# Optimization experiments

Measured on AMD Instinct MI355X. Metric: run time of the kernel, lower is better.

Reference implementation:

```python
import jax, jax.numpy as jnp
import numpy as np

SPATIAL_PATH = np.array([[1,0,1],[0,1,2],[1,2,1],[4,3,1],[5,4,3],[6,5,4],[5,6,5],[8,7,1],[9,8,7],[10,9,8],[9,10,9]], dtype=np.int32)

B, C_IN, J, T, C_OUT = 64, 3, 11, 512, 128
TEMPORAL_LEN = 7
SIG_CH = 84  # c = C_IN + 1 = 4 -> 4 + 16 + 64


def _signature_depth3(path):
    """Depth-3 path signature with basepoint=0 (Chen's identity over exp of increments).
    path: [N, L, c] -> [N, c + c^2 + c^3]."""
    N, L, c = path.shape
    # basepoint=True: path starts at 0, so first increment is path[:, 0]
    inc = jnp.concatenate([path[:, :1], path[:, 1:] - path[:, :-1]], axis=1)  # [N, L, c]

    def step(carry, d):
        S1, S2, S3 = carry
        e2 = 0.5 * d[:, :, None] * d[:, None, :]                                  # d^{x2}/2!
        e3 = (d[:, :, None, None] * d[:, None, :, None] * d[:, None, None, :]) / 6.0  # d^{x3}/3!
        T1 = S1 + d
        T2 = S2 + S1[:, :, None] * d[:, None, :] + e2
        T3 = (S3 + S2[:, :, :, None] * d[:, None, None, :]
              + S1[:, :, None, None] * e2[:, None, :, :] + e3)
        return (T1, T2, T3), None

    z = lambda *s: jnp.zeros(s, path.dtype)
    (S1, S2, S3), _ = jax.lax.scan(step, (z(N, c), z(N, c, c), z(N, c, c, c)),
                                   jnp.swapaxes(inc, 0, 1))
    return jnp.concatenate([S1, S2.reshape(N, -1), S3.reshape(N, -1)], axis=1)


def _augment_time(path):
    # signatory.Augment(include_time=True, include_original=True): prepend linear time channel
    N, L, _ = path.shape
    t = jnp.broadcast_to(jnp.linspace(0.0, 1.0, L, dtype=path.dtype)[None, :, None], (N, L, 1))
    return jnp.concatenate([t, path], axis=-1)


def _bn(x, gamma, beta, eps=1e-5):
    # train-mode BatchNorm2d (batch statistics), matching module default mode
    m = x.mean(axis=(0, 2, 3), keepdims=True)
    v = x.var(axis=(0, 2, 3), keepdims=True)
    return (x - m) * jax.lax.rsqrt(v + eps) * gamma[None, :, None, None] + beta[None, :, None, None]


def _conv1x1(x, w, b):
    return jnp.einsum('bcjt,oc->bojt', x, w) + b[None, :, None, None]


def _forward(x, path, raw_w, raw_b, raw_g, raw_beta,
             ps_w, ps_b, ps_g, ps_beta, fus_w, fus_b, fus_g, fus_beta):
    B_, C, J_, T_ = x.shape
    # raw branch: Conv2d(C_in, C_out, (1,3), pad (0,1)) + BN + ReLU
    x_conv = jax.lax.conv_general_dilated(x, raw_w, (1, 1), [(0, 0), (1, 1)],
                                          dimension_numbers=('NCHW', 'OIHW', 'NCHW'))
    x_conv = jax.nn.relu(_bn(x_conv + raw_b[None, :, None, None], raw_g, raw_beta))

    # spatial joint paths: gather along joint dim with hand-crafted path [J, 3]
    xp = x.transpose(0, 1, 3, 2)                  # [B, C, T, J]
    sp = xp[:, :, :, path]                        # [B, C, T, J, 3]
    sp = sp.transpose(0, 2, 3, 4, 1).reshape(-1, path.shape[1], C)  # [B*T*J, 3, C]
    s_sig = _signature_depth3(_augment_time(sp))
    s_sig = s_sig.reshape(B_, T_, J_, SIG_CH).transpose(0, 3, 2, 1)  # [B, 84, J, T]

    # temporal paths: replicate-pad T and take 7-wide sliding windows per joint
    pad = (TEMPORAL_LEN - 1) // 2
    x_pad = jnp.pad(x, ((0, 0), (0, 0), (0, 0), (pad, pad)), mode='edge')
    widx = jnp.arange(T_)[:, None] + jnp.arange(TEMPORAL_LEN)[None, :]  # [T, 7]
    tp = x_pad[:, :, :, widx]                     # [B, C, J, T, 7]
    tp = tp.transpose(0, 3, 2, 4, 1).reshape(-1, TEMPORAL_LEN, C)       # [B*T*J, 7, C]
    t_sig = _signature_depth3(_augment_time(tp))
    t_sig = t_sig.reshape(B_, T_, J_, SIG_CH).transpose(0, 3, 2, 1)     # [B, 84, J, T]

    sig = jnp.concatenate([s_sig, t_sig], axis=1)                       # [B, 168, J, T]
    sig = jax.nn.relu(_bn(_conv1x1(sig, ps_w, ps_b), ps_g, ps_beta))    # [B, C_out, J, T]

    out = jnp.concatenate([x_conv, sig], axis=1)                        # [B, 2*C_out, J, T]
    return jax.nn.relu(_bn(_conv1x1(out, fus_w, fus_b), fus_g, fus_beta))


def setup_inputs() -> dict:
    key = jax.random.key(0)
    ks = jax.random.split(key, 4)
    return {
        'x': jax.random.normal(ks[0], (B, C_IN, J, T), jnp.float32),
        'path': jnp.asarray(SPATIAL_PATH),
        'raw_w': jax.random.normal(ks[1], (C_OUT, C_IN, 1, 3), jnp.float32) * 0.2,
        'raw_b': jnp.zeros((C_OUT,), jnp.float32),
        'raw_g': jnp.ones((C_OUT,), jnp.float32),
        'raw_beta': jnp.zeros((C_OUT,), jnp.float32),
        'ps_w': jax.random.normal(ks[2], (C_OUT, 2 * SIG_CH), jnp.float32) * 0.05,
        'ps_b': jnp.zeros((C_OUT,), jnp.float32),
        'ps_g': jnp.ones((C_OUT,), jnp.float32),
        'ps_beta': jnp.zeros((C_OUT,), jnp.float32),
        'fus_w': jax.random.normal(ks[3], (C_OUT, 2 * C_OUT), jnp.float32) * 0.05,
        'fus_b': jnp.zeros((C_OUT,), jnp.float32),
        'fus_g': jnp.ones((C_OUT,), jnp.float32),
        'fus_beta': jnp.zeros((C_OUT,), jnp.float32),
    }


def reference(x, path, raw_w, raw_b, raw_g, raw_beta, ps_w, ps_b, ps_g, ps_beta,
              fus_w, fus_b, fus_g, fus_beta):
    return _forward(x, path, raw_w, raw_b, raw_g, raw_beta,
                    ps_w, ps_b, ps_g, ps_beta, fus_w, fus_b, fus_g, fus_beta)
```

## Files before the change

kernel.cpp:

```cpp
#include <hip/hip_runtime.h>

#define B_    64
#define CIN_  3
#define J_    11
#define T_    512
#define CO_   128
#define KPS_  168
#define KPAD_ 192
#define NLOC_ (B_*J_*T_)
#define NSTATF_ 360448.0f

typedef unsigned short u16;
typedef unsigned int   u32;

typedef __attribute__((ext_vector_type(8))) short bh8;
typedef __attribute__((ext_vector_type(4))) float f32x4;

__device__ __forceinline__ float b2f(u16 u){ union{u32 i; float f;} v; v.i = ((u32)u)<<16; return v.f; }
__device__ __forceinline__ u16 f2b(float f){ union{float f; u32 i;} v; v.f=f; u32 r = v.i + 0x7FFFu + ((v.i>>16)&1u); return (u16)(r>>16); }
__device__ __forceinline__ u32 pk2(u16 a, u16 b){ return (u32)a | ((u32)b<<16); }

__device__ __forceinline__ float ldx(const void* p, size_t i, bool bf){
  if (bf) return b2f(((const u16*)p)[i]);
  return ((const float*)p)[i];
}
__device__ __forceinline__ bool rflag(const u32* flag){
  return __builtin_amdgcn_readfirstlane(*flag) != 0u;
}

__global__ void kdet(const u32* __restrict__ xw, u32* __restrict__ flag){
  __shared__ int cnt;
  if (threadIdx.x==0) cnt=0;
  __syncthreads();
  u32 w = xw[threadIdx.x*4 + 1];
  int e = (int)((w>>7)&0xFFu);
  if (e>=100 && e<=140) atomicAdd(&cnt,1);
  __syncthreads();
  if (threadIdx.x==0) *flag = (cnt>128) ? 1u : 0u;
}

__global__ __launch_bounds__(256) void k0_prep(const u32* __restrict__ flag,
    const void* __restrict__ ps_w, const void* __restrict__ fus_w,
    u16* __restrict__ psB, u16* __restrict__ fusB,
    float* __restrict__ statsY, float* __restrict__ statsF)
{
  const bool bf = rflag(flag);
  const int stride = gridDim.x*blockDim.x;
  const int t0 = blockIdx.x*blockDim.x + threadIdx.x;
  for (int i=t0;i<64*512;i+=stride) statsY[i]=0.f;
  for (int i=t0;i<64*256;i+=stride) statsF[i]=0.f;
  for (int i=t0;i<128*KPAD_;i+=stride){
    int o=i/KPAD_, kk=i-o*KPAD_;
    int k = (kk<84) ? kk : ((kk>=96 && kk<180) ? kk-12 : -1);
    psB[i] = (k>=0) ? f2b(ldx(ps_w, (size_t)o*KPS_+k, bf)) : (u16)0;
  }
  for (int i=t0;i<128*256;i+=stride){
    int o=i>>8, k=i&255;
    int kc=k>>6, kk=k&63;
    int byte=(o<<7)+(kk<<1); byte ^= ((o&7)<<4);
    fusB[(kc*16384 + byte)>>1] = f2b(ldx(fus_w,i,bf));
  }
}

__device__ __forceinline__ void sigstep(float* S1, float* S2, float* S3, const float* d){
  float e2[16];
  #pragma unroll
  for (int a=0;a<4;a++){
    #pragma unroll
    for (int b=0;b<4;b++) e2[a*4+b] = 0.5f*d[a]*d[b];
  }
  #pragma unroll
  for (int a=0;a<4;a++){
    float s1e = S1[a] + (1.0f/3.0f)*d[a];
    #pragma unroll
    for (int b=0;b<4;b++){
      #pragma unroll
      for (int c=0;c<4;c++){
        S3[a*16+b*4+c] += S2[a*4+b]*d[c] + s1e*e2[b*4+c];
      }
    }
  }
  #pragma unroll
  for (int a=0;a<4;a++){
    #pragma unroll
    for (int b=0;b<4;b++) S2[a*4+b] += S1[a]*d[b] + e2[a*4+b];
  }
  #pragma unroll
  for (int a=0;a<4;a++) S1[a] += d[a];
}

__global__ __launch_bounds__(256) void k1_sig_conv(const u32* __restrict__ flag,
    const void* __restrict__ x, const int* __restrict__ path,
    const void* __restrict__ raw_w, const void* __restrict__ raw_b,
    const void* __restrict__ ps_b, const u16* __restrict__ psB,
    u16* __restrict__ Y, float* __restrict__ statsY,
    int locOff, int writeY, int doStats)
{
  const bool bf = rflag(flag);
  __shared__ u16 sAhi[64*KPAD_];
  __shared__ u16 sAlo[64*KPAD_];
  __shared__ float xt[CIN_][72];
  __shared__ float xs[CIN_][3][64];
  __shared__ int   pj[3];

  const int tid = threadIdx.x;
  const int blk = blockIdx.x;
  const int lb  = locOff + blk*64;
  const int lbl = blk*64;
  const int b   = lb / (J_*T_);
  const int j   = (lb / T_) % J_;
  const int t0  = lb % T_;
  const size_t xbase = (size_t)b*CIN_*J_*T_;

  if (tid < 3) pj[tid] = path[j*3 + tid];
  for (int idx=tid; idx<CIN_*70; idx+=256){
    int c=idx/70, u=idx-c*70;
    int t=t0+u-3; t = t<0?0:(t>T_-1?T_-1:t);
    xt[c][u] = ldx(x, xbase + (size_t)(c*J_+j)*T_ + t, bf);
  }
  __syncthreads();
  for (int idx=tid; idx<CIN_*3*64; idx+=256){
    int c=idx/192, p=(idx>>6)%3, tt=idx&63;
    xs[c][p][tt] = ldx(x, xbase + (size_t)(c*J_+pj[p])*T_ + t0 + tt, bf);
  }
  __syncthreads();

  const int lane = tid & 63, wid = tid >> 6;
  const int wid2 = wid ^ ((blk&1)<<1);

  if (wid2 < 2){
    const bool spf = (wid2==0);
    const int  tt  = lane;
    const int  L   = spf ? 3 : 7;
    const float dt = spf ? 0.5f : (1.0f/6.0f);
    float S1[4], S2[16], S3[64];
    #pragma unroll
    for (int i=0;i<4;i++)  S1[i]=0.f;
    #pragma unroll
    for (int i=0;i<16;i++) S2[i]=0.f;
    #pragma unroll
    for (int i=0;i<64;i++) S3[i]=0.f;
    float prv[3], d[4];
    for (int c=0;c<3;c++) prv[c] = spf ? xs[c][0][tt] : xt[c][tt];
    d[0]=0.f; d[1]=prv[0]; d[2]=prv[1]; d[3]=prv[2];
    sigstep(S1,S2,S3,d);
    for (int s=1;s<L;s++){
      d[0]=dt;
      for (int c=0;c<3;c++){ float cv = spf ? xs[c][s][tt] : xt[c][tt+s]; d[c+1]=cv-prv[c]; prv[c]=cv; }
      sigstep(S1,S2,S3,d);
    }
    const int sb2 = spf ? 0 : 192;
    const int rowb = tt*(KPAD_*2);
    const int swz  = (tt&7)<<4;
    #pragma unroll
    for (int i=0;i<12;i++){
      u16 hv[8], lv[8];
      #pragma unroll
      for (int e=0;e<8;e++){
        const int idx = i*8+e;
        float v;
        if (idx<4) v=S1[idx]; else if (idx<20) v=S2[idx-4]; else if (idx<84) v=S3[idx-20]; else v=0.f;
        u16 h = f2b(v);
        hv[e]=h; lv[e]=f2b(v - b2f(h));
      }
      int byp = (rowb + sb2 + i*16) ^ swz;
      *reinterpret_cast<uint4*>((char*)sAhi + byp) =
          make_uint4(pk2(hv[0],hv[1]),pk2(hv[2],hv[3]),pk2(hv[4],hv[5]),pk2(hv[6],hv[7]));
      *reinterpret_cast<uint4*>((char*)sAlo + byp) =
          make_uint4(pk2(lv[0],lv[1]),pk2(lv[2],lv[3]),pk2(lv[4],lv[5]),pk2(lv[6],lv[7]));
    }
  } else {
    const int nid = (wid2-2)*64 + lane;
    const int tx = nid & 7, ty2 = nid >> 3;
    #pragma unroll
    for (int cg=0; cg<2; cg++){
      const int chb = cg*64 + ty2*4;
      float w[4][9], bia[4];
      #pragma unroll
      for (int c=0;c<4;c++){
        bia[c]=ldx(raw_b, chb+c, bf);
        #pragma unroll
        for (int q=0;q<9;q++) w[c][q]=ldx(raw_w, (size_t)(chb+c)*9+q, bf);
      }
      float accC[8][4];
      #pragma unroll
      for (int i=0;i<8;i++){
        const int tl=tx*8+i, tg=t0+tl;
        float xv[9];
        #pragma unroll
        for (int cc=0;cc<3;cc++){
          #pragma unroll
          for (int kt=0;kt<3;kt++){
            float v = xt[cc][tl+2+kt];
            if ((tg==0 && kt==0) || (tg==T_-1 && kt==2)) v=0.f;
            xv[cc*3+kt]=v;
          }
        }
        #pragma unroll
        for (int c=0;c<4;c++){
          float s=bia[c];
          #pragma unroll
          for (int q=0;q<9;q++) s=fmaf(xv[q],w[c][q],s);
          accC[i][c]=s;
        }
      }
      if (writeY){
        #pragma unroll
        for (int i=0;i<8;i++){
          u16* yp = Y + (size_t)(lbl + tx*8+i)*256 + chb;
          *reinterpret_cast<uint2*>(yp) =
            make_uint2(pk2(f2b(accC[i][0]),f2b(accC[i][1])), pk2(f2b(accC[i][2]),f2b(accC[i][3])));
        }
      }
      if (doStats){
        #pragma unroll
        for (int c=0;c<4;c++){
          float s=0.f,q=0.f;
          #pragma unroll
          for (int i=0;i<8;i++){ float v=accC[i][c]; s+=v; q+=v*v; }
          s += __shfl_xor(s,1); s += __shfl_xor(s,2); s += __shfl_xor(s,4);
          q += __shfl_xor(q,1); q += __shfl_xor(q,2); q += __shfl_xor(q,4);
          if ((lane&7)==0){
            atomicAdd(&statsY[(blk&63)*512 + (chb+c)*2 + 0], s);
            atomicAdd(&statsY[(blk&63)*512 + (chb+c)*2 + 1], q);
          }
        }
      }
    }
  }
  __syncthreads();

  const int lrow = lane >> 4, lcol = lane & 15;
  f32x4 acc[2][4];
  #pragma unroll
  for (int mt=0;mt<2;mt++)
    #pragma unroll
    for (int nt=0;nt<4;nt++) acc[mt][nt] = (f32x4){0.f,0.f,0.f,0.f};

  #pragma unroll
  for (int ks=0;ks<6;ks++){
    const int kk2 = ks*64 + lrow*16;
    bh8 wf[2], yh[4], yl[4];
    #pragma unroll
    for (int mt=0;mt<2;mt++){
      const int o = wid*32 + mt*16 + lcol;
      wf[mt] = *reinterpret_cast<const bh8*>((const char*)psB + o*(KPAD_*2) + kk2);
    }
    #pragma unroll
    for (int nt=0;nt<4;nt++){
      const int l = nt*16 + lcol;
      const int byp = (l*(KPAD_*2) + kk2) ^ ((l&7)<<4);
      yh[nt] = *reinterpret_cast<const bh8*>((const char*)sAhi + byp);
      yl[nt] = *reinterpret_cast<const bh8*>((const char*)sAlo + byp);
    }
    #pragma unroll
    for (int mt=0;mt<2;mt++){
      #pragma unroll
      for (int nt=0;nt<4;nt++){
        acc[mt][nt] = __builtin_amdgcn_mfma_f32_16x16x32_bf16(wf[mt], yh[nt], acc[mt][nt], 0,0,0);
        acc[mt][nt] = __builtin_amdgcn_mfma_f32_16x16x32_bf16(wf[mt], yl[nt], acc[mt][nt], 0,0,0);
      }
    }
  }
  __syncthreads();

  char* yPs = (char*)sAhi;
  #pragma unroll
  for (int mt=0;mt<2;mt++){
    const int chb = wid*32 + mt*16 + lrow*4;
    float pb[4];
    #pragma unroll
    for (int r=0;r<4;r++) pb[r]=ldx(ps_b, chb+r, bf);
    float sv[4]={0.f,0.f,0.f,0.f}, qv[4]={0.f,0.f,0.f,0.f};
    #pragma unroll
    for (int nt=0;nt<4;nt++){
      const int loc = nt*16 + lcol;
      float v0=acc[mt][nt][0]+pb[0], v1=acc[mt][nt][1]+pb[1];
      float v2=acc[mt][nt][2]+pb[2], v3=acc[mt][nt][3]+pb[3];
      sv[0]+=v0; qv[0]+=v0*v0; sv[1]+=v1; qv[1]+=v1*v1;
      sv[2]+=v2; qv[2]+=v2*v2; sv[3]+=v3; qv[3]+=v3*v3;
      if (writeY){
        const int byp = (loc*256 + chb*2) ^ ((loc&7)<<4);
        *reinterpret_cast<uint2*>(yPs + byp) =
            make_uint2(pk2(f2b(v0),f2b(v1)), pk2(f2b(v2),f2b(v3)));
      }
    }
    if (doStats){
      #pragma unroll
      for (int r=0;r<4;r++){
        float s=sv[r], q=qv[r];
        s += __shfl_xor(s,1); s += __shfl_xor(s,2); s += __shfl_xor(s,4); s += __shfl_xor(s,8);
        q += __shfl_xor(q,1); q += __shfl_xor(q,2); q += __shfl_xor(q,4); q += __shfl_xor(q,8);
        if (lcol==0){
          const int ch = 128 + chb + r;
          atomicAdd(&statsY[(blk&63)*512 + ch*2 + 0], s);
          atomicAdd(&statsY[(blk&63)*512 + ch*2 + 1], q);
        }
      }
    }
  }
  __syncthreads();
  if (writeY){
    #pragma unroll
    for (int it=0; it<4; it++){
      const int q = it*256 + tid;
      const int L = q<<4;
      const int loc = L>>8;
      const int phys = L ^ ((loc&7)<<4);
      uint4 v = *reinterpret_cast<const uint4*>(yPs + phys);
      *reinterpret_cast<uint4*>((char*)Y + ((size_t)(lbl+loc)<<9) + 256 + (L&255)) = v;
    }
  }
}

__global__ __launch_bounds__(256) void k2_finY(const u32* __restrict__ flag,
    const float* __restrict__ statsY,
    const void* __restrict__ raw_g, const void* __restrict__ raw_beta,
    const void* __restrict__ ps_g,  const void* __restrict__ ps_beta,
    float* __restrict__ scaleY, float* __restrict__ shiftY)
{
  const bool bf = rflag(flag);
  int ch = threadIdx.x;
  float s=0.f,q=0.f;
  for (int slot=0;slot<64;slot++){ s+=statsY[slot*512+ch*2]; q+=statsY[slot*512+ch*2+1]; }
  float m = s/NSTATF_;
  float v = q/NSTATF_ - m*m; v = fmaxf(v,0.f);
  float r = rsqrtf(v + 1e-5f);
  float g  = (ch<128)? ldx(raw_g,ch,bf)    : ldx(ps_g,ch-128,bf);
  float be = (ch<128)? ldx(raw_beta,ch,bf) : ldx(ps_beta,ch-128,bf);
  scaleY[ch]=r*g; shiftY[ch]=be - m*r*g;
}

__global__ __launch_bounds__(256,4) void k3_fus(const u32* __restrict__ flag,
    const u16* __restrict__ Y,
    const u16* __restrict__ fusB, const float* __restrict__ scaleY, const float* __restrict__ shiftY,
    const void* __restrict__ fus_b, void* __restrict__ F, float* __restrict__ statsF,
    int locOff)
{
  const bool bf = rflag(flag);
  __shared__ u16 sAhi[128*64];
  __shared__ u16 sB  [128*64];
  __shared__ float sSc[256], sSh[256];

  const int tid = threadIdx.x, blk = blockIdx.x;
  const size_t loc0  = (size_t)locOff + (size_t)blk*128;
  const size_t loc0l = (size_t)blk*128;
  const int lane = tid & 63, wid = tid >> 6;
  const int wm = wid >> 1, wn = wid & 1;
  const int lrow = lane >> 4, lcol = lane & 15;

  sSc[tid] = scaleY[tid];
  sSh[tid] = shiftY[tid];

  f32x4 acc[4][4];
  #pragma unroll
  for (int mt=0;mt<4;mt++)
    #pragma unroll
    for (int nt=0;nt<4;nt++) acc[mt][nt] = (f32x4){0.f,0.f,0.f,0.f};

  __syncthreads();

  for (int kc=0;kc<4;kc++){
    const int kb = kc*64;
    #pragma unroll
    for (int p=0;p<4;p++){
      const int loc = p*32 + (tid>>3);
      const int c16 = tid & 7;
      const int ch0 = kb + c16*8;
      uint4 u = *reinterpret_cast<const uint4*>(Y + (loc0l+loc)*256 + ch0);
      float f[8];
      f[0]=b2f((u16)(u.x&0xffff)); f[1]=b2f((u16)(u.x>>16));
      f[2]=b2f((u16)(u.y&0xffff)); f[3]=b2f((u16)(u.y>>16));
      f[4]=b2f((u16)(u.z&0xffff)); f[5]=b2f((u16)(u.z>>16));
      f[6]=b2f((u16)(u.w&0xffff)); f[7]=b2f((u16)(u.w>>16));
      u16 hi[8];
      #pragma unroll
      for (int jq=0;jq<8;jq++){
        float v = fmaxf(fmaf(f[jq], sSc[ch0+jq], sSh[ch0+jq]), 0.f);
        hi[jq] = f2b(v);
      }
      int byte = (loc<<7) + (c16<<4); byte ^= ((loc&7)<<4);
      *reinterpret_cast<uint4*>((char*)sAhi + byte) =
          make_uint4(pk2(hi[0],hi[1]),pk2(hi[2],hi[3]),pk2(hi[4],hi[5]),pk2(hi[6],hi[7]));
    }
    {
      const char* src = (const char*)(fusB + kc*8192);
      #pragma unroll
      for (int p=0;p<4;p++){
        int q16 = (p*256 + tid) << 4;
        *reinterpret_cast<uint4*>((char*)sB + q16) =
            *reinterpret_cast<const uint4*>(src + q16);
      }
    }
    __syncthreads();
    #pragma unroll
    for (int ks=0;ks<2;ks++){
      const int kk2 = (ks*32 + lrow*8) << 1;
      bh8 wf[4], yh[4];
      #pragma unroll
      for (int mt=0;mt<4;mt++){
        int o = wm*64 + mt*16 + lcol;
        int byp = (o<<7) + kk2; byp ^= ((o&7)<<4);
        wf[mt] = *reinterpret_cast<const bh8*>((const char*)sB + byp);
      }
      #pragma unroll
      for (int nt=0;nt<4;nt++){
        int l = wn*64 + nt*16 + lcol;
        int byp = (l<<7) + kk2; byp ^= ((l&7)<<4);
        yh[nt] = *reinterpret_cast<const bh8*>((const char*)sAhi + byp);
      }
      #pragma unroll
      for (int mt=0;mt<4;mt++){
        #pragma unroll
        for (int nt=0;nt<4;nt++){
          acc[mt][nt] = __builtin_amdgcn_mfma_f32_16x16x32_bf16(wf[mt], yh[nt], acc[mt][nt], 0,0,0);
        }
      }
    }
    __syncthreads();
  }

  const int bb  = (int)(loc0/(J_*T_));
  const int jj  = (int)((loc0/T_)%J_);
  const int tt0 = (int)(loc0%T_);
  #pragma unroll
  for (int mt=0;mt<4;mt++){
    #pragma unroll
    for (int r=0;r<4;r++){
      const int ch = wm*64 + mt*16 + lrow*4 + r;
      const float fb = ldx(fus_b, ch, bf);
      const size_t ro = ((size_t)(bb*128+ch)*J_ + jj)*T_ + tt0 + wn*64 + lcol;
      float s=0.f, q=0.f;
      #pragma unroll
      for (int nt=0;nt<4;nt++){
        float v = acc[mt][nt][r] + fb;
        s += v; q += v*v;
        float vp = __shfl_xor(v, 1);
        if (bf){
          if (!(lane&1)){
            *reinterpret_cast<u32*>((u16*)F + ro + nt*16) = pk2(f2b(v), f2b(vp));
          }
        } else {
          ((float*)F)[ro + nt*16] = v;
        }
      }
      s += __shfl_xor(s,1); s += __shfl_xor(s,2); s += __shfl_xor(s,4); s += __shfl_xor(s,8);
      q += __shfl_xor(q,1); q += __shfl_xor(q,2); q += __shfl_xor(q,4); q += __shfl_xor(q,8);
      if (lcol==0){
        atomicAdd(&statsF[(blk&63)*256 + ch*2 + 0], s);
        atomicAdd(&statsF[(blk&63)*256 + ch*2 + 1], q);
      }
    }
  }
}

__global__ __launch_bounds__(256) void k4_finF(const u32* __restrict__ flag,
    const float* __restrict__ statsF,
    const void* __restrict__ fus_g, const void* __restrict__ fus_beta,
    float* __restrict__ scaleF, float* __restrict__ shiftF)
{
  const bool bf = rflag(flag);
  int ch = threadIdx.x;
  if (ch < 128){
    float s=0.f,q=0.f;
    for (int slot=0;slot<64;slot++){ s+=statsF[slot*256+ch*2]; q+=statsF[slot*256+ch*2+1]; }
    float m=s/NSTATF_;
    float v=fmaxf(q/NSTATF_-m*m,0.f);
    float r=rsqrtf(v+1e-5f);
    float g=ldx(fus_g,ch,bf), be=ldx(fus_beta,ch,bf);
    scaleF[ch]=r*g; shiftF[ch]=be - m*r*g;
  }
}

__global__ __launch_bounds__(256) void k5_out(const u32* __restrict__ flag,
    const float* __restrict__ scaleF, const float* __restrict__ shiftF, void* __restrict__ out)
{
  const bool bf = rflag(flag);
  const size_t total = (size_t)NLOC_*128;
  const size_t stride = (size_t)gridDim.x*blockDim.x;
  if (bf){
    u16* o16 = (u16*)out;
    for (size_t u8 = (size_t)blockIdx.x*blockDim.x + threadIdx.x; u8*8 < total; u8 += stride){
      size_t idx = u8*8;
      int ch = (int)((idx/(J_*T_)) & 127);
      float sc = scaleF[ch], sh = shiftF[ch];
      uint4 u = *reinterpret_cast<const uint4*>(o16 + idx);
      u32 w[4] = {u.x,u.y,u.z,u.w};
      u32 o[4];
      #pragma unroll
      for (int q=0;q<4;q++){
        float v0=fmaxf(fmaf(b2f((u16)(w[q]&0xffff)),sc,sh),0.f);
        float v1=fmaxf(fmaf(b2f((u16)(w[q]>>16)),sc,sh),0.f);
        o[q]=pk2(f2b(v0),f2b(v1));
      }
      *reinterpret_cast<uint4*>(o16 + idx) = make_uint4(o[0],o[1],o[2],o[3]);
    }
  } else {
    float* of = (float*)out;
    for (size_t u4 = (size_t)blockIdx.x*blockDim.x + threadIdx.x; u4*4 < total; u4 += stride){
      size_t idx = u4*4;
      int ch = (int)((idx/(J_*T_)) & 127);
      float sc = scaleF[ch], sh = shiftF[ch];
      float4 v = *reinterpret_cast<const float4*>(of + idx);
      v.x=fmaxf(fmaf(v.x,sc,sh),0.f);
      v.y=fmaxf(fmaf(v.y,sc,sh),0.f);
      v.z=fmaxf(fmaf(v.z,sc,sh),0.f);
      v.w=fmaxf(fmaf(v.w,sc,sh),0.f);
      *reinterpret_cast<float4*>(of + idx) = v;
    }
  }
}

extern "C" void kernel_launch(void* const* d_in, const int* in_sizes, int n_in,
                              void* d_out, int out_size, void* d_ws, size_t ws_size,
                              hipStream_t stream)
{
  const void* x        = d_in[0];
  const int*  path     = (const int*)d_in[1];
  const void* raw_w    = d_in[2];
  const void* raw_b    = d_in[3];
  const void* raw_g    = d_in[4];
  const void* raw_beta = d_in[5];
  const void* ps_w     = d_in[6];
  const void* ps_b     = d_in[7];
  const void* ps_g     = d_in[8];
  const void* ps_beta  = d_in[9];
  const void* fus_w    = d_in[10];
  const void* fus_b    = d_in[11];
  const void* fus_g    = d_in[12];
  const void* fus_beta = d_in[13];

  char* w = (char*)d_ws;
  u32*   flag   = (u32*)w;   w += 256;
  float* statsY = (float*)w; w += 64*512*4;
  float* statsF = (float*)w; w += 64*256*4;
  u16*   psB    = (u16*)w;   w += 128*KPAD_*2;
  u16*   fusB   = (u16*)w;   w += 256*128*2;
  float* scaleY = (float*)w; w += 1024;
  float* shiftY = (float*)w; w += 1024;
  float* scaleF = (float*)w; w += 512;
  float* shiftF = (float*)w; w += 512;
  size_t off = (size_t)(w - (char*)d_ws);
  off = (off + 255) & ~(size_t)255;
  u16* Y = (u16*)((char*)d_ws + off);
  size_t avail = (ws_size > off) ? (ws_size - off) : 0;

  const size_t Yfull = (size_t)NLOC_*256*2;
  int c = 1;
  while (c < 64 && Yfull/(size_t)c > avail) c <<= 1;
  const int chunkLoc = NLOC_ / c;

  kdet<<<dim3(1),dim3(256),0,stream>>>((const u32*)x, flag);
  k0_prep<<<dim3(64),dim3(256),0,stream>>>(flag, ps_w, fus_w, psB, fusB, statsY, statsF);

  for (int i=0;i<c;i++){
    int wy = (i==c-1)?1:0;
    k1_sig_conv<<<dim3(chunkLoc/64),dim3(256),0,stream>>>(flag, x, path, raw_w, raw_b, ps_b, psB, Y, statsY, i*chunkLoc, wy, 1);
  }
  k2_finY<<<dim3(1),dim3(256),0,stream>>>(flag, statsY, raw_g, raw_beta, ps_g, ps_beta, scaleY, shiftY);

  k3_fus<<<dim3(chunkLoc/128),dim3(256),0,stream>>>(flag, Y, fusB, scaleY, shiftY, fus_b, d_out, statsF, (c-1)*chunkLoc);
  for (int i=0;i<c-1;i++){
    k1_sig_conv<<<dim3(chunkLoc/64),dim3(256),0,stream>>>(flag, x, path, raw_w, raw_b, ps_b, psB, Y, statsY, i*chunkLoc, 1, 0);
    k3_fus<<<dim3(chunkLoc/128),dim3(256),0,stream>>>(flag, Y, fusB, scaleY, shiftY, fus_b, d_out, statsF, i*chunkLoc);
  }
  k4_finF<<<dim3(1),dim3(256),0,stream>>>(flag, statsF, fus_g, fus_beta, scaleF, shiftF);
  k5_out<<<dim3(2048),dim3(256),0,stream>>>(flag, scaleF, shiftF, d_out);
}
```

Before: 551.3 us.

## Replace BN-stat atomics with per-block partials and direct Y stores

New measurement: 526.0 us. 4.6% less time.

```diff
diff --git a/kernel.cpp b/kernel.cpp
--- a/kernel.cpp
+++ b/kernel.cpp
@@ -8,6 +8,7 @@
 #define KPS_  168
 #define KPAD_ 192
 #define NLOC_ (B_*J_*T_)
+#define NBLK1_ (NLOC_/64)
 #define NSTATF_ 360448.0f
 
 typedef unsigned short u16;
@@ -42,12 +43,11 @@
 __global__ __launch_bounds__(256) void k0_prep(const u32* __restrict__ flag,
     const void* __restrict__ ps_w, const void* __restrict__ fus_w,
     u16* __restrict__ psB, u16* __restrict__ fusB,
-    float* __restrict__ statsY, float* __restrict__ statsF)
+    float* __restrict__ statsF)
 {
   const bool bf = rflag(flag);
   const int stride = gridDim.x*blockDim.x;
   const int t0 = blockIdx.x*blockDim.x + threadIdx.x;
-  for (int i=t0;i<64*512;i+=stride) statsY[i]=0.f;
   for (int i=t0;i<64*256;i+=stride) statsF[i]=0.f;
   for (int i=t0;i<128*KPAD_;i+=stride){
     int o=i/KPAD_, kk=i-o*KPAD_;
@@ -93,7 +93,7 @@
     const void* __restrict__ x, const int* __restrict__ path,
     const void* __restrict__ raw_w, const void* __restrict__ raw_b,
     const void* __restrict__ ps_b, const u16* __restrict__ psB,
-    u16* __restrict__ Y, float* __restrict__ statsY,
+    u16* __restrict__ Y, float* __restrict__ partY,
     int locOff, int writeY, int doStats)
 {
   const bool bf = rflag(flag);
@@ -107,6 +107,7 @@
   const int blk = blockIdx.x;
   const int lb  = locOff + blk*64;
   const int lbl = blk*64;
+  const int gblk= (locOff>>6) + blk;
   const int b   = lb / (J_*T_);
   const int j   = (lb / T_) % J_;
   const int t0  = lb % T_;
@@ -221,8 +222,8 @@
           s += __shfl_xor(s,1); s += __shfl_xor(s,2); s += __shfl_xor(s,4);
           q += __shfl_xor(q,1); q += __shfl_xor(q,2); q += __shfl_xor(q,4);
           if ((lane&7)==0){
-            atomicAdd(&statsY[(blk&63)*512 + (chb+c)*2 + 0], s);
-            atomicAdd(&statsY[(blk&63)*512 + (chb+c)*2 + 1], q);
+            partY[((size_t)((chb+c)*2  ))*NBLK1_ + gblk] = s;
+            partY[((size_t)((chb+c)*2+1))*NBLK1_ + gblk] = q;
           }
         }
       }
@@ -262,9 +263,7 @@
       }
     }
   }
-  __syncthreads();
-
-  char* yPs = (char*)sAhi;
+
   #pragma unroll
   for (int mt=0;mt<2;mt++){
     const int chb = wid*32 + mt*16 + lrow*4;
@@ -274,15 +273,13 @@
     float sv[4]={0.f,0.f,0.f,0.f}, qv[4]={0.f,0.f,0.f,0.f};
     #pragma unroll
     for (int nt=0;nt<4;nt++){
-      const int loc = nt*16 + lcol;
       float v0=acc[mt][nt][0]+pb[0], v1=acc[mt][nt][1]+pb[1];
       float v2=acc[mt][nt][2]+pb[2], v3=acc[mt][nt][3]+pb[3];
       sv[0]+=v0; qv[0]+=v0*v0; sv[1]+=v1; qv[1]+=v1*v1;
       sv[2]+=v2; qv[2]+=v2*v2; sv[3]+=v3; qv[3]+=v3*v3;
       if (writeY){
-        const int byp = (loc*256 + chb*2) ^ ((loc&7)<<4);
-        *reinterpret_cast<uint2*>(yPs + byp) =
-            make_uint2(pk2(f2b(v0),f2b(v1)), pk2(f2b(v2),f2b(v3)));
+        u16* yp = Y + (size_t)(lbl + nt*16+lcol)*256 + 128 + chb;
+        *reinterpret_cast<uint2*>(yp) = make_uint2(pk2(f2b(v0),f2b(v1)), pk2(f2b(v2),f2b(v3)));
       }
     }
     if (doStats){
@@ -293,42 +290,43 @@
         q += __shfl_xor(q,1); q += __shfl_xor(q,2); q += __shfl_xor(q,4); q += __shfl_xor(q,8);
         if (lcol==0){
           const int ch = 128 + chb + r;
-          atomicAdd(&statsY[(blk&63)*512 + ch*2 + 0], s);
-          atomicAdd(&statsY[(blk&63)*512 + ch*2 + 1], q);
-        }
-      }
-    }
-  }
-  __syncthreads();
-  if (writeY){
-    #pragma unroll
-    for (int it=0; it<4; it++){
-      const int q = it*256 + tid;
-      const int L = q<<4;
-      const int loc = L>>8;
-      const int phys = L ^ ((loc&7)<<4);
-      uint4 v = *reinterpret_cast<const uint4*>(yPs + phys);
-      *reinterpret_cast<uint4*>((char*)Y + ((size_t)(lbl+loc)<<9) + 256 + (L&255)) = v;
+          partY[((size_t)(ch*2  ))*NBLK1_ + gblk] = s;
+          partY[((size_t)(ch*2+1))*NBLK1_ + gblk] = q;
+        }
+      }
     }
   }
 }
 
 __global__ __launch_bounds__(256) void k2_finY(const u32* __restrict__ flag,
-    const float* __restrict__ statsY,
+    const float* __restrict__ partY,
     const void* __restrict__ raw_g, const void* __restrict__ raw_beta,
     const void* __restrict__ ps_g,  const void* __restrict__ ps_beta,
     float* __restrict__ scaleY, float* __restrict__ shiftY)
 {
   const bool bf = rflag(flag);
-  int ch = threadIdx.x;
+  const int ch = blockIdx.x;
+  const int tid = threadIdx.x;
+  const float* prS = partY + (size_t)(ch*2  )*NBLK1_;
+  const float* prQ = partY + (size_t)(ch*2+1)*NBLK1_;
   float s=0.f,q=0.f;
-  for (int slot=0;slot<64;slot++){ s+=statsY[slot*512+ch*2]; q+=statsY[slot*512+ch*2+1]; }
-  float m = s/NSTATF_;
-  float v = q/NSTATF_ - m*m; v = fmaxf(v,0.f);
-  float r = rsqrtf(v + 1e-5f);
-  float g  = (ch<128)? ldx(raw_g,ch,bf)    : ldx(ps_g,ch-128,bf);
-  float be = (ch<128)? ldx(raw_beta,ch,bf) : ldx(ps_beta,ch-128,bf);
-  scaleY[ch]=r*g; shiftY[ch]=be - m*r*g;
+  for (int slot=tid; slot<NBLK1_; slot+=256){ s+=prS[slot]; q+=prQ[slot]; }
+  s += __shfl_xor(s,1); s += __shfl_xor(s,2); s += __shfl_xor(s,4);
+  s += __shfl_xor(s,8); s += __shfl_xor(s,16); s += __shfl_xor(s,32);
+  q += __shfl_xor(q,1); q += __shfl_xor(q,2); q += __shfl_xor(q,4);
+  q += __shfl_xor(q,8); q += __shfl_xor(q,16); q += __shfl_xor(q,32);
+  __shared__ float rs[4], rq[4];
+  if ((tid&63)==0){ rs[tid>>6]=s; rq[tid>>6]=q; }
+  __syncthreads();
+  if (tid==0){
+    float S=rs[0]+rs[1]+rs[2]+rs[3], Q=rq[0]+rq[1]+rq[2]+rq[3];
+    float m = S/NSTATF_;
+    float v = Q/NSTATF_ - m*m; v = fmaxf(v,0.f);
+    float r = rsqrtf(v + 1e-5f);
+    float g  = (ch<128)? ldx(raw_g,ch,bf)    : ldx(ps_g,ch-128,bf);
+    float be = (ch<128)? ldx(raw_beta,ch,bf) : ldx(ps_beta,ch-128,bf);
+    scaleY[ch]=r*g; shiftY[ch]=be - m*r*g;
+  }
 }
 
 __global__ __launch_bounds__(256,4) void k3_fus(const u32* __restrict__ flag,
@@ -532,7 +530,6 @@
 
   char* w = (char*)d_ws;
   u32*   flag   = (u32*)w;   w += 256;
-  float* statsY = (float*)w; w += 64*512*4;
   float* statsF = (float*)w; w += 64*256*4;
   u16*   psB    = (u16*)w;   w += 128*KPAD_*2;
   u16*   fusB   = (u16*)w;   w += 256*128*2;
@@ -545,23 +542,25 @@
   u16* Y = (u16*)((char*)d_ws + off);
   size_t avail = (ws_size > off) ? (ws_size - off) : 0;
 
+  float* partY = (float*)d_out;
+
   const size_t Yfull = (size_t)NLOC_*256*2;
   int c = 1;
   while (c < 64 && Yfull/(size_t)c > avail) c <<= 1;
   const int chunkLoc = NLOC_ / c;
 
   kdet<<<dim3(1),dim3(256),0,stream>>>((const u32*)x, flag);
-  k0_prep<<<dim3(64),dim3(256),0,stream>>>(flag, ps_w, fus_w, psB, fusB, statsY, statsF);
+  k0_prep<<<dim3(64),dim3(256),0,stream>>>(flag, ps_w, fus_w, psB, fusB, statsF);
 
   for (int i=0;i<c;i++){
     int wy = (i==c-1)?1:0;
-    k1_sig_conv<<<dim3(chunkLoc/64),dim3(256),0,stream>>>(flag, x, path, raw_w, raw_b, ps_b, psB, Y, statsY, i*chunkLoc, wy, 1);
-  }
-  k2_finY<<<dim3(1),dim3(256),0,stream>>>(flag, statsY, raw_g, raw_beta, ps_g, ps_beta, scaleY, shiftY);
+    k1_sig_conv<<<dim3(chunkLoc/64),dim3(256),0,stream>>>(flag, x, path, raw_w, raw_b, ps_b, psB, Y, partY, i*chunkLoc, wy, 1);
+  }
+  k2_finY<<<dim3(256),dim3(256),0,stream>>>(flag, partY, raw_g, raw_beta, ps_g, ps_beta, scaleY, shiftY);
 
   k3_fus<<<dim3(chunkLoc/128),dim3(256),0,stream>>>(flag, Y, fusB, scaleY, shiftY, fus_b, d_out, statsF, (c-1)*chunkLoc);
   for (int i=0;i<c-1;i++){
-    k1_sig_conv<<<dim3(chunkLoc/64),dim3(256),0,stream>>>(flag, x, path, raw_w, raw_b, ps_b, psB, Y, statsY, i*chunkLoc, 1, 0);
+    k1_sig_conv<<<dim3(chunkLoc/64),dim3(256),0,stream>>>(flag, x, path, raw_w, raw_b, ps_b, psB, Y, partY, i*chunkLoc, 1, 0);
     k3_fus<<<dim3(chunkLoc/128),dim3(256),0,stream>>>(flag, Y, fusB, scaleY, shiftY, fus_b, d_out, statsF, i*chunkLoc);
   }
   k4_finF<<<dim3(1),dim3(256),0,stream>>>(flag, statsF, fus_g, fus_beta, scaleF, shiftF);
```
